# Optimization experiments

Measured on AMD Instinct MI355X. Metric: run time of the kernel, lower is better.

The kernel has to match this reference:

```python
import jax, jax.numpy as jnp
import numpy as np

IN_FEATURES = 512
OUT_FEATURES = 128
KERNEL_DIM = 32
BATCH = 128


def setup_inputs() -> dict:
    key = jax.random.key(0)
    kx, kT = jax.random.split(key)
    x = jax.random.normal(kx, (BATCH, IN_FEATURES), dtype=jnp.float32)
    # nn.Parameter initialized with normal(0, 1)
    T = jax.random.normal(kT, (IN_FEATURES, OUT_FEATURES, KERNEL_DIM), dtype=jnp.float32)
    return {"x": x, "T": T}


def reference(x, T):
    B = x.shape[0]
    in_f, out_f, k_dim = T.shape
    # projection: [B, in] @ [in, out*k] -> [B, out, k]
    m = (x @ T.reshape(in_f, out_f * k_dim)).reshape(B, out_f, k_dim)
    # pairwise L1 distance over kernel dim: [B, B, out]
    # original: M = m[None], M_T = m[:, None]; norm = |M - M_T|.sum(3); o_b = exp(-norm).sum(0) - 1
    norm = jnp.abs(m[None, :, :, :] - m[:, None, :, :]).sum(axis=-1)  # [i=B, j=B, out]
    o_b = jnp.exp(-norm).sum(axis=0) - 1.0  # [B, out] (subtract self-distance term exp(0)=1)
    return jnp.concatenate([x, o_b], axis=1)  # [B, in + out]
```

## Files before the change

### kernel.cpp

```cpp
#include <hip/hip_runtime.h>

#define IN_F    512
#define NC      4096
#define OUT_COLS 640
#define AS_PITCH 136
#define MO_PITCH 36
#define BK      128

typedef __attribute__((ext_vector_type(8))) short  bf16x8;
typedef __attribute__((ext_vector_type(4))) float  f32x4;

static __device__ __forceinline__ unsigned short f2bfu(float f) {
    return (unsigned short)(__float_as_uint(f) >> 16);
}
static __device__ __forceinline__ unsigned int pack2(float lo, float hi) {
    return (__float_as_uint(lo) >> 16) | (__float_as_uint(hi) & 0xFFFF0000u);
}

__global__ __launch_bounds__(1024, 4) void fused_kernel(
    const float* __restrict__ x,
    const float* __restrict__ T,
    float* __restrict__ out)
{
    __shared__ __align__(16) char smem[51968];
    unsigned short* as = (unsigned short*)smem;
    unsigned short* bs = (unsigned short*)(smem + 34816);
    float* mo   = (float*)smem;
    float* psum = (float*)(smem + 43520);

    const int tid   = threadIdx.x;
    const int lane  = tid & 63;
    const int w     = tid >> 6;
    const int col   = lane & 15;
    const int q     = lane >> 4;
    const int o     = blockIdx.x >> 1;
    const int jhalf = blockIdx.x & 1;
    const int mt    = w >> 1;
    const int nt    = w & 1;

    if (tid < 64) {
        int idx = blockIdx.x * 64 + tid;
        int b = idx >> 7, c4 = idx & 127;
        float4 v = ((const float4*)x)[idx];
        *(float4*)(out + b * OUT_COLS + c4 * 4) = v;
    }

    f32x4 acc = {0.f, 0.f, 0.f, 0.f};
    for (int k0 = 0; k0 < IN_F; k0 += BK) {
        __syncthreads();
        #pragma unroll
        for (int p = 0; p < 4; ++p) {
            int u   = tid + p * 1024;
            int row = u >> 5, c4 = u & 31;
            float4 v = *(const float4*)(x + row * IN_F + k0 + c4 * 4);
            uint2 pv;
            pv.x = pack2(v.x, v.y); pv.y = pack2(v.z, v.w);
            *(uint2*)(as + row * AS_PITCH + c4 * 4) = pv;
        }
        {
            int kk = tid >> 3, cq = tid & 7;
            float4 v = *(const float4*)(T + (size_t)(k0 + kk) * NC + o * 32 + cq * 4);
            int nb = cq * 4;
            bs[(nb + 0) * AS_PITCH + kk] = f2bfu(v.x);
            bs[(nb + 1) * AS_PITCH + kk] = f2bfu(v.y);
            bs[(nb + 2) * AS_PITCH + kk] = f2bfu(v.z);
            bs[(nb + 3) * AS_PITCH + kk] = f2bfu(v.w);
        }
        __syncthreads();
        #pragma unroll
        for (int kt = 0; kt < 4; ++kt) {
            const int krel = kt * 32 + q * 8;
            bf16x8 af  = *(const bf16x8*)(as + (mt * 16 + col) * AS_PITCH + krel);
            bf16x8 bfr = *(const bf16x8*)(bs + (nt * 16 + col) * AS_PITCH + krel);
            acc = __builtin_amdgcn_mfma_f32_16x16x32_bf16(af, bfr, acc, 0, 0, 0);
        }
    }
    __syncthreads();
    {
        float* dst = mo + (size_t)(mt * 16 + q * 4) * MO_PITCH + nt * 16 + col;
        dst[0 * MO_PITCH] = acc[0]; dst[1 * MO_PITCH] = acc[1];
        dst[2 * MO_PITCH] = acc[2]; dst[3 * MO_PITCH] = acc[3];
    }
    __syncthreads();

    const int jj5 = tid & 31;
    const int isl = tid >> 5;
    const int j0  = jhalf * 64 + jj5;

    float mj0[32], mj1[32];
    #pragma unroll
    for (int k4 = 0; k4 < 8; ++k4) {
        float4 a = *(const float4*)(mo + (size_t)j0 * MO_PITCH + k4 * 4);
        float4 b = *(const float4*)(mo + (size_t)(j0 + 32) * MO_PITCH + k4 * 4);
        mj0[k4*4+0] = a.x; mj0[k4*4+1] = a.y; mj0[k4*4+2] = a.z; mj0[k4*4+3] = a.w;
        mj1[k4*4+0] = b.x; mj1[k4*4+1] = b.y; mj1[k4*4+2] = b.z; mj1[k4*4+3] = b.w;
    }

    float s0 = 0.f, s1 = 0.f;
    #pragma unroll
    for (int ii = 0; ii < 4; ++ii) {
        const int i = isl * 4 + ii;
        float n0 = 0.f, n1 = 0.f;
        #pragma unroll
        for (int k4 = 0; k4 < 8; ++k4) {
            float4 v = *(const float4*)(mo + (size_t)i * MO_PITCH + k4 * 4);
            n0 += fabsf(mj0[k4*4+0] - v.x) + fabsf(mj0[k4*4+1] - v.y)
                + fabsf(mj0[k4*4+2] - v.z) + fabsf(mj0[k4*4+3] - v.w);
            n1 += fabsf(mj1[k4*4+0] - v.x) + fabsf(mj1[k4*4+1] - v.y)
                + fabsf(mj1[k4*4+2] - v.z) + fabsf(mj1[k4*4+3] - v.w);
        }
        s0 += __expf(-n0);
        s1 += __expf(-n1);
    }
    psum[jj5 * 33 + isl]        = s0;
    psum[1056 + jj5 * 33 + isl] = s1;
    __syncthreads();
    if (tid < 64) {
        int jsel = tid >> 5, jj = tid & 31;
        float tot = 0.f;
        #pragma unroll
        for (int u = 0; u < 32; ++u) tot += psum[jsel * 1056 + jj * 33 + u];
        out[(jhalf * 64 + jsel * 32 + jj) * OUT_COLS + IN_F + o] = tot - 1.0f;
    }
}

extern "C" void kernel_launch(void* const* d_in, const int* in_sizes, int n_in,
                              void* d_out, int out_size, void* d_ws, size_t ws_size,
                              hipStream_t stream) {
    const float* x = (const float*)d_in[0];
    const float* T = (const float*)d_in[1];
    float* out = (float*)d_out;
    (void)d_ws; (void)ws_size;

    fused_kernel<<<256, 1024, 0, stream>>>(x, T, out);
}
```

Baseline: 75.98 us.

## Split fused kernel into prep, T-convert, GEMM and pairwise kernels

Result: slower. 80.73 us (+6.3%).

```diff
diff --git a/kernel.cpp b/kernel.cpp
--- a/kernel.cpp
+++ b/kernel.cpp
@@ -3,9 +3,8 @@
 #define IN_F    512
 #define NC      4096
 #define OUT_COLS 640
-#define AS_PITCH 136
-#define MO_PITCH 36
-#define BK      128
+#define B_SZ    128
+#define KD      32
 
 typedef __attribute__((ext_vector_type(8))) short  bf16x8;
 typedef __attribute__((ext_vector_type(4))) float  f32x4;
@@ -17,93 +16,103 @@
     return (__float_as_uint(lo) >> 16) | (__float_as_uint(hi) & 0xFFFF0000u);
 }
 
-__global__ __launch_bounds__(1024, 4) void fused_kernel(
-    const float* __restrict__ x,
-    const float* __restrict__ T,
+__global__ __launch_bounds__(256) void prep_kernel(
+    const float* __restrict__ x, float* __restrict__ out,
+    unsigned short* __restrict__ xa)
+{
+    const int g = blockIdx.x * 256 + threadIdx.x;
+    {
+        int b = g >> 7, c4 = g & 127;
+        float4 v = ((const float4*)x)[g];
+        *(float4*)(out + b * OUT_COLS + c4 * 4) = v;
+    }
+    const int s = g >> 1, half = g & 1;
+    const int mt = s >> 10, kt = (s >> 6) & 15, lane = s & 63;
+    const int col = lane & 15, q = lane >> 4;
+    float4 v = *(const float4*)(x + (mt * 16 + col) * IN_F + kt * 32 + q * 8 + half * 4);
+    uint2 pv; pv.x = pack2(v.x, v.y); pv.y = pack2(v.z, v.w);
+    *(uint2*)(xa + (size_t)s * 8 + half * 4) = pv;
+}
+
+__global__ __launch_bounds__(256) void prepT_kernel(
+    const float* __restrict__ T, unsigned short* __restrict__ tb)
+{
+    const int s = blockIdx.x * 256 + threadIdx.x;
+    const int nt = s >> 10, kt = (s >> 6) & 15, lane = s & 63;
+    const int col = lane & 15, q = lane >> 4;
+    const float* src = T + (size_t)(kt * 32 + q * 8) * NC + nt * 16 + col;
+    float b0 = src[0*NC], b1 = src[1*NC], b2 = src[2*NC], b3 = src[3*NC];
+    float b4 = src[4*NC], b5 = src[5*NC], b6 = src[6*NC], b7 = src[7*NC];
+    uint4 pv;
+    pv.x = pack2(b0, b1); pv.y = pack2(b2, b3);
+    pv.z = pack2(b4, b5); pv.w = pack2(b6, b7);
+    *(uint4*)(tb + (size_t)s * 8) = pv;
+}
+
+__global__ __launch_bounds__(256) void gemm_kernel(
+    const unsigned short* __restrict__ xa,
+    const unsigned short* __restrict__ tb,
+    float* __restrict__ m)
+{
+    const int tid  = threadIdx.x;
+    const int lane = tid & 63;
+    const int w    = tid >> 6;
+    const int t    = blockIdx.x * 4 + w;
+    const int nt   = t >> 3, mt = t & 7;
+    const int col  = lane & 15, q = lane >> 4;
+
+    f32x4 acc = {0.f, 0.f, 0.f, 0.f};
+    const unsigned short* pa = xa + (size_t)(mt * 16) * 512 + lane * 8;
+    const unsigned short* pb = tb + (size_t)(nt * 16) * 512 + lane * 8;
+    #pragma unroll 8
+    for (int kt = 0; kt < 16; ++kt) {
+        bf16x8 af  = *(const bf16x8*)(pa + (size_t)kt * 512);
+        bf16x8 bfr = *(const bf16x8*)(pb + (size_t)kt * 512);
+        acc = __builtin_amdgcn_mfma_f32_16x16x32_bf16(af, bfr, acc, 0, 0, 0);
+    }
+    const int n = nt * 16 + col, o = n >> 5, nk = n & 31;
+    float* dst = m + (size_t)o * (B_SZ * KD) + (mt * 16 + q * 4) * KD + nk;
+    dst[0 * KD] = acc[0]; dst[1 * KD] = acc[1];
+    dst[2 * KD] = acc[2]; dst[3 * KD] = acc[3];
+}
+
+__global__ __launch_bounds__(512) void pairwise_kernel(
+    const float* __restrict__ m,
     float* __restrict__ out)
 {
-    __shared__ __align__(16) char smem[51968];
-    unsigned short* as = (unsigned short*)smem;
-    unsigned short* bs = (unsigned short*)(smem + 34816);
-    float* mo   = (float*)smem;
-    float* psum = (float*)(smem + 43520);
+    __shared__ float mo[B_SZ * KD];
+    __shared__ float psum[2 * 32 * 17];
 
     const int tid   = threadIdx.x;
-    const int lane  = tid & 63;
-    const int w     = tid >> 6;
-    const int col   = lane & 15;
-    const int q     = lane >> 4;
     const int o     = blockIdx.x >> 1;
     const int jhalf = blockIdx.x & 1;
-    const int mt    = w >> 1;
-    const int nt    = w & 1;
 
-    if (tid < 64) {
-        int idx = blockIdx.x * 64 + tid;
-        int b = idx >> 7, c4 = idx & 127;
-        float4 v = ((const float4*)x)[idx];
-        *(float4*)(out + b * OUT_COLS + c4 * 4) = v;
-    }
-
-    f32x4 acc = {0.f, 0.f, 0.f, 0.f};
-    for (int k0 = 0; k0 < IN_F; k0 += BK) {
-        __syncthreads();
-        #pragma unroll
-        for (int p = 0; p < 4; ++p) {
-            int u   = tid + p * 1024;
-            int row = u >> 5, c4 = u & 31;
-            float4 v = *(const float4*)(x + row * IN_F + k0 + c4 * 4);
-            uint2 pv;
-            pv.x = pack2(v.x, v.y); pv.y = pack2(v.z, v.w);
-            *(uint2*)(as + row * AS_PITCH + c4 * 4) = pv;
-        }
-        {
-            int kk = tid >> 3, cq = tid & 7;
-            float4 v = *(const float4*)(T + (size_t)(k0 + kk) * NC + o * 32 + cq * 4);
-            int nb = cq * 4;
-            bs[(nb + 0) * AS_PITCH + kk] = f2bfu(v.x);
-            bs[(nb + 1) * AS_PITCH + kk] = f2bfu(v.y);
-            bs[(nb + 2) * AS_PITCH + kk] = f2bfu(v.z);
-            bs[(nb + 3) * AS_PITCH + kk] = f2bfu(v.w);
-        }
-        __syncthreads();
-        #pragma unroll
-        for (int kt = 0; kt < 4; ++kt) {
-            const int krel = kt * 32 + q * 8;
-            bf16x8 af  = *(const bf16x8*)(as + (mt * 16 + col) * AS_PITCH + krel);
-            bf16x8 bfr = *(const bf16x8*)(bs + (nt * 16 + col) * AS_PITCH + krel);
-            acc = __builtin_amdgcn_mfma_f32_16x16x32_bf16(af, bfr, acc, 0, 0, 0);
-        }
-    }
-    __syncthreads();
-    {
-        float* dst = mo + (size_t)(mt * 16 + q * 4) * MO_PITCH + nt * 16 + col;
-        dst[0 * MO_PITCH] = acc[0]; dst[1 * MO_PITCH] = acc[1];
-        dst[2 * MO_PITCH] = acc[2]; dst[3 * MO_PITCH] = acc[3];
-    }
+    const float4* src = (const float4*)(m + (size_t)o * (B_SZ * KD));
+    ((float4*)mo)[tid]       = src[tid];
+    ((float4*)mo)[tid + 512] = src[tid + 512];
     __syncthreads();
 
     const int jj5 = tid & 31;
     const int isl = tid >> 5;
     const int j0  = jhalf * 64 + jj5;
 
-    float mj0[32], mj1[32];
+    float mj0[KD], mj1[KD];
     #pragma unroll
     for (int k4 = 0; k4 < 8; ++k4) {
-        float4 a = *(const float4*)(mo + (size_t)j0 * MO_PITCH + k4 * 4);
-        float4 b = *(const float4*)(mo + (size_t)(j0 + 32) * MO_PITCH + k4 * 4);
+        float4 a = *(const float4*)(m + (size_t)o * (B_SZ * KD) + j0 * KD + k4 * 4);
+        float4 b = *(const float4*)(m + (size_t)o * (B_SZ * KD) + (j0 + 32) * KD + k4 * 4);
         mj0[k4*4+0] = a.x; mj0[k4*4+1] = a.y; mj0[k4*4+2] = a.z; mj0[k4*4+3] = a.w;
         mj1[k4*4+0] = b.x; mj1[k4*4+1] = b.y; mj1[k4*4+2] = b.z; mj1[k4*4+3] = b.w;
     }
 
     float s0 = 0.f, s1 = 0.f;
     #pragma unroll
-    for (int ii = 0; ii < 4; ++ii) {
-        const int i = isl * 4 + ii;
+    for (int ii = 0; ii < 8; ++ii) {
+        const int i = isl * 8 + ii;
         float n0 = 0.f, n1 = 0.f;
         #pragma unroll
         for (int k4 = 0; k4 < 8; ++k4) {
-            float4 v = *(const float4*)(mo + (size_t)i * MO_PITCH + k4 * 4);
+            float4 v = ((const float4*)mo)[i * 8 + k4];
             n0 += fabsf(mj0[k4*4+0] - v.x) + fabsf(mj0[k4*4+1] - v.y)
                 + fabsf(mj0[k4*4+2] - v.z) + fabsf(mj0[k4*4+3] - v.w);
             n1 += fabsf(mj1[k4*4+0] - v.x) + fabsf(mj1[k4*4+1] - v.y)
@@ -112,14 +121,14 @@
         s0 += __expf(-n0);
         s1 += __expf(-n1);
     }
-    psum[jj5 * 33 + isl]        = s0;
-    psum[1056 + jj5 * 33 + isl] = s1;
+    psum[jj5 * 17 + isl]       = s0;
+    psum[544 + jj5 * 17 + isl] = s1;
     __syncthreads();
     if (tid < 64) {
         int jsel = tid >> 5, jj = tid & 31;
         float tot = 0.f;
         #pragma unroll
-        for (int u = 0; u < 32; ++u) tot += psum[jsel * 1056 + jj * 33 + u];
+        for (int u = 0; u < 16; ++u) tot += psum[jsel * 544 + jj * 17 + u];
         out[(jhalf * 64 + jsel * 32 + jj) * OUT_COLS + IN_F + o] = tot - 1.0f;
     }
 }
@@ -130,7 +139,12 @@
     const float* x = (const float*)d_in[0];
     const float* T = (const float*)d_in[1];
     float* out = (float*)d_out;
-    (void)d_ws; (void)ws_size;
+    float* m = (float*)d_ws;
+    unsigned short* xa = (unsigned short*)((char*)d_ws + (2u << 20));
+    unsigned short* tb = (unsigned short*)((char*)d_ws + (2u << 20) + (128u << 10));
 
-    fused_kernel<<<256, 1024, 0, stream>>>(x, T, out);
+    prep_kernel<<<64, 256, 0, stream>>>(x, out, xa);
+    prepT_kernel<<<1024, 256, 0, stream>>>(T, tb);
+    gemm_kernel<<<512, 256, 0, stream>>>(xa, tb, m);
+    pairwise_kernel<<<256, 512, 0, stream>>>(m, out);
 }
```
